# Kernel optimization log

Measured on AMD Instinct MI355X. Metric: run time of the kernel, lower is better.

The kernel has to match this reference:

```python
import jax, jax.numpy as jnp
import numpy as np

# ---- configuration (matches init_kwargs) ----
B, C_IO, T = 2, 64, 4096
PATCH = 2
W0, W1 = 512, 1024           # widths
D_DN, D_MID = 2, 4           # depths per level
DH = 64                      # dim per head
WIN = 128                    # local attention window
MAP = 1024                   # mapping_dim
DFF_MAP = 1024               # mapping_d_ff
FF_MULT = 2                  # GEGLU ff_mult in local levels
H_DN = W0 // DH              # 8 heads
H_MID = W1 // DH             # 16 heads


def _n(key, shape, s=0.02):
    return jax.random.normal(key, shape, jnp.float32) * s


def setup_inputs() -> dict:
    key = jax.random.key(0)
    ks = iter(jax.random.split(key, 64))
    p = {}
    p['x'] = jax.random.normal(next(ks), (B, C_IO, T), jnp.float32)
    p['t'] = jax.random.uniform(next(ks), (B,), jnp.float32)
    p['time_w'] = jax.random.normal(next(ks), (MAP // 2, 1), jnp.float32)
    p['time_in_w'] = _n(next(ks), (MAP, MAP))
    p['map_in_s'] = jnp.ones((MAP,), jnp.float32)
    p['map_norm_s'] = jnp.ones((2, MAP), jnp.float32)
    p['map_up_w'] = _n(next(ks), (2, MAP, 2 * DFF_MAP))
    p['map_down_w'] = _n(next(ks), (2, DFF_MAP, MAP))
    p['map_out_s'] = jnp.ones((MAP,), jnp.float32)
    p['patch_in_w'] = _n(next(ks), (C_IO * PATCH, W0))
    p['dn_anorm_w'] = _n(next(ks), (D_DN, MAP, W0))
    p['dn_qkv_w'] = _n(next(ks), (D_DN, W0, 3 * W0))
    p['dn_o_w'] = _n(next(ks), (D_DN, W0, W0))
    p['dn_fnorm_w'] = _n(next(ks), (D_DN, MAP, W0))
    p['dn_ff1_w'] = _n(next(ks), (D_DN, W0, 2 * FF_MULT * W0))
    p['dn_ff2_w'] = _n(next(ks), (D_DN, FF_MULT * W0, W0))
    p['merge_w'] = _n(next(ks), (W0 * 2, W1))
    p['mid_map_w'] = _n(next(ks), (MAP, W1))
    p['mid_pin_w'] = _n(next(ks), (W1, W1))
    p['mid_pout_w'] = _n(next(ks), (W1, W1))
    p['mid_ln1_g'] = jnp.ones((D_MID, W1), jnp.float32)
    p['mid_ln1_b'] = jnp.zeros((D_MID, W1), jnp.float32)
    p['mid_qkv_w'] = _n(next(ks), (D_MID, W1, 3 * W1))
    p['mid_o_w'] = _n(next(ks), (D_MID, W1, W1))
    p['mid_ln2_g'] = jnp.ones((D_MID, W1), jnp.float32)
    p['mid_ln2_b'] = jnp.zeros((D_MID, W1), jnp.float32)
    p['mid_ff1_w'] = _n(next(ks), (D_MID, W1, 8 * W1))
    p['mid_ff2_w'] = _n(next(ks), (D_MID, 4 * W1, W1))
    p['mid_fn_g'] = jnp.ones((W1,), jnp.float32)
    p['mid_fn_b'] = jnp.zeros((W1,), jnp.float32)
    p['split_w'] = _n(next(ks), (W1, W0 * 2))
    p['split_fac'] = jnp.full((1,), 0.5, jnp.float32)
    p['up_anorm_w'] = _n(next(ks), (D_DN, MAP, W0))
    p['up_qkv_w'] = _n(next(ks), (D_DN, W0, 3 * W0))
    p['up_o_w'] = _n(next(ks), (D_DN, W0, W0))
    p['up_fnorm_w'] = _n(next(ks), (D_DN, MAP, W0))
    p['up_ff1_w'] = _n(next(ks), (D_DN, W0, 2 * FF_MULT * W0))
    p['up_ff2_w'] = _n(next(ks), (D_DN, FF_MULT * W0, W0))
    p['out_norm_s'] = jnp.ones((W0,), jnp.float32)
    p['patch_out_w'] = _n(next(ks), (W0, C_IO * PATCH))
    return p


def rmsnorm(x, scale, eps=1e-6):
    ms = jnp.mean(jnp.square(x), -1, keepdims=True)
    return x * (scale * jax.lax.rsqrt(ms + eps))


def layernorm(x, g, b, eps=1e-5):
    m = jnp.mean(x, -1, keepdims=True)
    v = jnp.mean(jnp.square(x - m), -1, keepdims=True)
    return (x - m) * jax.lax.rsqrt(v + eps) * g + b


def rope_tables(S, D):
    inv = 1.0 / (10000.0 ** (jnp.arange(0, D, 2, dtype=jnp.float32) / D))
    ang = jnp.arange(S, dtype=jnp.float32)[:, None] * inv  # [S, D/2]
    return jnp.cos(ang), jnp.sin(ang)


def apply_rope(x, cos, sin):
    # x: [B,H,S,D], contiguous-half rotation
    x1, x2 = jnp.split(x, 2, -1)
    return jnp.concatenate([x1 * cos - x2 * sin, x2 * cos + x1 * sin], -1)


def heads_split(x, h):
    Bx, S, C = x.shape
    return x.reshape(Bx, S, h, C // h).transpose(0, 2, 1, 3)


def heads_merge(x):
    Bx, h, S, D = x.shape
    return x.transpose(0, 2, 1, 3).reshape(Bx, S, h * D)


def local_attn(q, k, v, w):
    # non-causal sliding-window attention: each query window attends to
    # [prev, self, next] windows (look_backward=1, look_forward=1)
    Bx, H, S, D = q.shape
    nw = S // w
    qw = q.reshape(Bx, H, nw, w, D)
    def ctx(tn):
        tw = tn.reshape(Bx, H, nw, w, D)
        pad = jnp.pad(tw, ((0, 0), (0, 0), (1, 1), (0, 0), (0, 0)))
        return jnp.concatenate([pad[:, :, :-2], pad[:, :, 1:-1], pad[:, :, 2:]], 3)  # [B,H,nw,3w,D]
    kw, vw = ctx(k), ctx(v)
    s = jnp.einsum('bhnqd,bhnkd->bhnqk', qw * (D ** -0.5), kw)
    valid = jnp.ones((nw, 3 * w), bool).at[0, :w].set(False).at[-1, 2 * w:].set(False)
    s = jnp.where(valid[None, None, :, None, :], s, jnp.finfo(s.dtype).min)
    a = jax.nn.softmax(s, -1)
    return jnp.einsum('bhnqk,bhnkd->bhnqd', a, vw).reshape(Bx, H, S, D)


def token_merge(x, w, r=2):
    # 'b (n r) c -> b n (c r)' then linear
    Bx, S, C = x.shape
    x = x.reshape(Bx, S // r, r, C).transpose(0, 1, 3, 2).reshape(Bx, S // r, C * r)
    return x @ w


def token_split(x, w, r=2):
    # linear then 'b n (c r) -> b (n r) c'
    y = x @ w
    Bx, n, CR = y.shape
    C = CR // r
    return y.reshape(Bx, n, C, r).transpose(0, 1, 3, 2).reshape(Bx, n * r, C)


def mapping(e, in_s, norm_s, up_w, down_w, out_s):
    x = rmsnorm(e, in_s)
    for l in range(up_w.shape[0]):
        h = rmsnorm(x, norm_s[l])
        a, g = jnp.split(h @ up_w[l], 2, -1)
        x = x + (a * jax.nn.gelu(g)) @ down_w[l]
    return rmsnorm(x, out_s)


def local_level(x, cond, anorm, qkv_w, o_w, fnorm, ff1, ff2, heads, win):
    Bx, S, C = x.shape
    D = C // heads
    cos, sin = rope_tables(S, D)
    for l in range(qkv_w.shape[0]):
        h = rmsnorm(x, 1.0 + (cond @ anorm[l])[:, None, :])  # AdaRMSNorm
        q, k, v = jnp.split(h @ qkv_w[l], 3, -1)
        q, k, v = heads_split(q, heads), heads_split(k, heads), heads_split(v, heads)
        q, k = apply_rope(q, cos, sin), apply_rope(k, cos, sin)
        x = x + heads_merge(local_attn(q, k, v, win)) @ o_w[l]
        h = rmsnorm(x, 1.0 + (cond @ fnorm[l])[:, None, :])
        a, g = jnp.split(h @ ff1[l], 2, -1)
        x = x + (a * jax.nn.gelu(g)) @ ff2[l]  # GEGLU FF
    return x


def mid_level(x, ln1g, ln1b, qkv_w, o_w, ln2g, ln2b, ff1, ff2, fng, fnb, heads):
    Bx, S, C = x.shape
    D = C // heads
    cos, sin = rope_tables(S, D)
    for l in range(qkv_w.shape[0]):
        h = layernorm(x, ln1g[l], ln1b[l])
        q, k, v = jnp.split(h @ qkv_w[l], 3, -1)
        q, k, v = heads_split(q, heads), heads_split(k, heads), heads_split(v, heads)
        q, k = apply_rope(q, cos, sin), apply_rope(k, cos, sin)
        s = jnp.einsum('bhqd,bhkd->bhqk', q * (D ** -0.5), k)
        o = jnp.einsum('bhqk,bhkd->bhqd', jax.nn.softmax(s, -1), v)
        x = x + heads_merge(o) @ o_w[l]
        h = layernorm(x, ln2g[l], ln2b[l])
        a, g = jnp.split(h @ ff1[l], 2, -1)
        x = x + (a * jax.nn.silu(g)) @ ff2[l]  # SwiGLU FF
    return layernorm(x, fng, fnb)


def _forward(x, t, time_w, time_in_w, map_in_s, map_norm_s, map_up_w, map_down_w, map_out_s,
             patch_in_w, dn_anorm_w, dn_qkv_w, dn_o_w, dn_fnorm_w, dn_ff1_w, dn_ff2_w,
             merge_w, mid_map_w, mid_pin_w, mid_pout_w, mid_ln1_g, mid_ln1_b, mid_qkv_w,
             mid_o_w, mid_ln2_g, mid_ln2_b, mid_ff1_w, mid_ff2_w, mid_fn_g, mid_fn_b,
             split_w, split_fac, up_anorm_w, up_qkv_w, up_o_w, up_fnorm_w, up_ff1_w,
             up_ff2_w, out_norm_s, patch_out_w):
    h = jnp.swapaxes(x, 1, 2)                      # [B,T,C_io]
    h = token_merge(h, patch_in_w, PATCH)          # [B, T/2, W0]
    f = 2.0 * jnp.pi * (t[:, None] @ time_w.T)     # Fourier features
    temb = jnp.concatenate([jnp.cos(f), jnp.sin(f)], -1) @ time_in_w
    cond = mapping(temb, map_in_s, map_norm_s, map_up_w, map_down_w, map_out_s)  # [B,MAP]
    h = local_level(h, cond, dn_anorm_w, dn_qkv_w, dn_o_w, dn_fnorm_w, dn_ff1_w, dn_ff2_w, H_DN, WIN)
    skip = h
    h = token_merge(h, merge_w)                    # [B, T/4, W1]
    h = h @ mid_pin_w
    pre = (cond @ mid_map_w)[:, None, :]           # prepended mapping token
    h = jnp.concatenate([pre, h], 1)
    h = mid_level(h, mid_ln1_g, mid_ln1_b, mid_qkv_w, mid_o_w, mid_ln2_g, mid_ln2_b,
                  mid_ff1_w, mid_ff2_w, mid_fn_g, mid_fn_b, H_MID)
    h = (h @ mid_pout_w)[:, 1:, :]
    h = token_split(h, split_w)                    # back to [B, T/2, W0]
    h = skip + split_fac * (h - skip)              # lerp skip fusion
    h = local_level(h, cond, up_anorm_w, up_qkv_w, up_o_w, up_fnorm_w, up_ff1_w, up_ff2_w, H_DN, WIN)
    h = rmsnorm(h, out_norm_s)
    h = token_split(h, patch_out_w, PATCH)         # [B,T,C_io]
    return jnp.swapaxes(h, 1, 2)


def reference(x, t, time_w, time_in_w, map_in_s, map_norm_s, map_up_w, map_down_w, map_out_s,
              patch_in_w, dn_anorm_w, dn_qkv_w, dn_o_w, dn_fnorm_w, dn_ff1_w, dn_ff2_w,
              merge_w, mid_map_w, mid_pin_w, mid_pout_w, mid_ln1_g, mid_ln1_b, mid_qkv_w,
              mid_o_w, mid_ln2_g, mid_ln2_b, mid_ff1_w, mid_ff2_w, mid_fn_g, mid_fn_b,
              split_w, split_fac, up_anorm_w, up_qkv_w, up_o_w, up_fnorm_w, up_ff1_w,
              up_ff2_w, out_norm_s, patch_out_w):
    return _forward(x, t, time_w, time_in_w, map_in_s, map_norm_s, map_up_w, map_down_w, map_out_s,
                    patch_in_w, dn_anorm_w, dn_qkv_w, dn_o_w, dn_fnorm_w, dn_ff1_w, dn_ff2_w,
                    merge_w, mid_map_w, mid_pin_w, mid_pout_w, mid_ln1_g, mid_ln1_b, mid_qkv_w,
                    mid_o_w, mid_ln2_g, mid_ln2_b, mid_ff1_w, mid_ff2_w, mid_fn_g, mid_fn_b,
                    split_w, split_fac, up_anorm_w, up_qkv_w, up_o_w, up_fnorm_w, up_ff1_w,
                    up_ff2_w, out_norm_s, patch_out_w)
```

## Files before the change

### kernel.cpp

```cpp
#include <hip/hip_runtime.h>
#include <math.h>

#define BB   2
#define CIO  64
#define TT   4096
#define S0   2048
#define W0   512
#define HDN  8
#define SM   1025
#define SMP  1088
#define W1   1024
#define HMID 16
#define WIN  128
#define NW   16
#define MAPD 1024
#define KSPL 16
#define PKCAP 8396800L

typedef _Float16 f16;
typedef _Float16 half8 __attribute__((ext_vector_type(8)));
typedef _Float16 half4v __attribute__((ext_vector_type(4)));
typedef _Float16 half2v __attribute__((ext_vector_type(2)));
typedef float floatx4 __attribute__((ext_vector_type(4)));

__device__ __forceinline__ float gelu_tanh(float x) {
    float x3 = x * x * x;
    return 0.5f * x * (1.f + tanhf(0.7978845608028654f * (x + 0.044715f * x3)));
}

__global__ __launch_bounds__(256) void wcast(
    const float* __restrict__ W, f16* __restrict__ Wt, int K, int N) {
    __shared__ float T[64][65];
    const int n0 = blockIdx.x * 64, k0 = blockIdx.y * 64;
    const int tid = threadIdx.x;
    for (int e = tid; e < 4096; e += 256) {
        int r = e >> 6, c = e & 63;
        T[r][c] = W[(size_t)(k0 + r) * N + n0 + c];
    }
    __syncthreads();
    for (int e = tid; e < 2048; e += 256) {
        int r = e >> 5, c2 = (e & 31) * 2;
        half2v p;
        p[0] = (f16)T[c2][r];
        p[1] = (f16)T[c2 + 1][r];
        *(half2v*)(Wt + (size_t)(n0 + r) * K + k0 + c2) = p;
    }
}

template<int OUTM>
__global__ __launch_bounds__(256) void gemm_h(
    const f16* __restrict__ A, const f16* __restrict__ Bt,
    const float* __restrict__ res, void* __restrict__ Cv,
    int M, int N, int K) {
    __shared__ __align__(16) f16 As[3][4096];
    __shared__ __align__(16) f16 Bs[3][4096];
    const int tid = threadIdx.x;
    const int wv = tid >> 6, ln = tid & 63;
    int nwg = gridDim.x * gridDim.y;
    int orig = blockIdx.y * gridDim.x + blockIdx.x;
    int wg = orig;
    if (nwg >= 16) {
        int q = nwg >> 3, r = nwg & 7;
        int xcd = orig & 7, lot = orig >> 3;
        wg = (xcd < r ? xcd * (q + 1) : r * (q + 1) + (xcd - r) * q) + lot;
    }
    const int bm = (wg / gridDim.x) * 128, bn = (wg % gridDim.x) * 128;
    int Kc = K, kbase = 0;
    if (OUTM == 2) { Kc = K / gridDim.z; kbase = blockIdx.z * Kc; }
    const int nt = Kc >> 5;

    auto stage = [&](int buf, int kt) {
        int k0 = kbase + (kt << 5);
#pragma unroll
        for (int i = 0; i < 2; ++i) {
            int off = i * 4096 + wv * 1024 + ln * 16;
            int row = off >> 6, kb = (off & 63) >> 1;
            int gr = bm + row; gr = gr < M ? gr : M - 1;
            f16* gp = const_cast<f16*>(A) + (size_t)gr * K + k0 + kb;
            __builtin_amdgcn_global_load_lds(
                (__attribute__((address_space(1))) void*)gp,
                (__attribute__((address_space(3))) void*)(&As[buf][i * 2048 + wv * 512]),
                16, 0, 0);
            f16* gq = const_cast<f16*>(Bt) + (size_t)(bn + row) * K + k0 + kb;
            __builtin_amdgcn_global_load_lds(
                (__attribute__((address_space(1))) void*)gq,
                (__attribute__((address_space(3))) void*)(&Bs[buf][i * 2048 + wv * 512]),
                16, 0, 0);
        }
    };

    floatx4 acc[4][4];
#pragma unroll
    for (int m = 0; m < 4; ++m)
#pragma unroll
        for (int n = 0; n < 4; ++n) acc[m][n] = (floatx4)0.f;
    const int r = ln & 15, kc = (ln >> 4) * 8;
    const int wr = (wv >> 1) * 64, wc = (wv & 1) * 64;

    stage(0, 0);
    if (nt > 1) stage(1, 1);
    int buf = 0;
    for (int t = 0; t < nt; ++t) {
        if (t + 1 < nt) { asm volatile("s_waitcnt vmcnt(4)" ::: "memory"); }
        else            { asm volatile("s_waitcnt vmcnt(0)" ::: "memory"); }
        __builtin_amdgcn_s_barrier();
        if (t + 2 < nt) {
            int nb = buf + 2; if (nb >= 3) nb -= 3;
            stage(nb, t + 2);
        }
        half8 af[4], bf[4];
#pragma unroll
        for (int m = 0; m < 4; ++m)
            af[m] = *(const half8*)(&As[buf][(wr + m * 16 + r) * 32 + kc]);
#pragma unroll
        for (int n = 0; n < 4; ++n)
            bf[n] = *(const half8*)(&Bs[buf][(wc + n * 16 + r) * 32 + kc]);
#pragma unroll
        for (int m = 0; m < 4; ++m)
#pragma unroll
            for (int n = 0; n < 4; ++n)
                acc[m][n] = __builtin_amdgcn_mfma_f32_16x16x32_f16(af[m], bf[n], acc[m][n], 0, 0, 0);
        if (++buf >= 3) buf = 0;
    }

    float* Cf = (float*)Cv;
    f16*   Ch = (f16*)Cv;
    if (OUTM == 2) Cf += (size_t)blockIdx.z * M * N;
#pragma unroll
    for (int m = 0; m < 4; ++m) {
        int rbase = bm + wr + m * 16 + ((ln >> 4) << 2);
#pragma unroll
        for (int j = 0; j < 4; ++j) {
            int row = rbase + j;
            if (row < M) {
                size_t ro = (size_t)row * N;
#pragma unroll
                for (int n = 0; n < 4; ++n) {
                    int col = bn + wc + n * 16 + (ln & 15);
                    float v = acc[m][n][j];
                    if (OUTM == 1) Ch[ro + col] = (f16)v;
                    else if (OUTM == 0) Cf[ro + col] = v + (res ? res[ro + col] : 0.f);
                    else Cf[ro + col] = v;
                }
            }
        }
    }
}

template<bool HOUT>
__global__ __launch_bounds__(256) void kred(
    const float* __restrict__ P, const float* __restrict__ res,
    void* __restrict__ Cv, size_t mn, int ks) {
    size_t i = ((size_t)blockIdx.x * 256 + threadIdx.x) * 4;
    if (i >= mn) return;
    floatx4 s = res ? *(const floatx4*)(res + i) : (floatx4)0.f;
    for (int z = 0; z < ks; ++z) {
        floatx4 p = *(const floatx4*)(P + (size_t)z * mn + i);
        s += p;
    }
    if (HOUT) {
        half4v h;
#pragma unroll
        for (int j = 0; j < 4; ++j) h[j] = (f16)s[j];
        *(half4v*)((f16*)Cv + i) = h;
    } else {
        *(floatx4*)((float*)Cv + i) = s;
    }
}

__global__ __launch_bounds__(256) void gemv2_part(
    const float* __restrict__ A, const float* __restrict__ W,
    float* __restrict__ P, int N, int K) {
    int n = blockIdx.x * 256 + threadIdx.x;
    if (n >= N) return;
    int Kc = K / KSPL;
    int k0 = blockIdx.y * Kc;
    float acc0 = 0.f, acc1 = 0.f;
    const float* Wp = W + (size_t)k0 * N + n;
    const float* a0 = A + k0;
    const float* a1 = A + K + k0;
#pragma unroll 4
    for (int k = 0; k < Kc; ++k) {
        float w = Wp[(size_t)k * N];
        acc0 = fmaf(a0[k], w, acc0);
        acc1 = fmaf(a1[k], w, acc1);
    }
    P[((size_t)blockIdx.y * 2 + 0) * N + n] = acc0;
    P[((size_t)blockIdx.y * 2 + 1) * N + n] = acc1;
}

__global__ __launch_bounds__(256) void gemv2_red(
    const float* __restrict__ P, const float* __restrict__ res,
    float* __restrict__ C, int N) {
    int g = blockIdx.x * 256 + threadIdx.x;
    if (g >= 2 * N) return;
    int m = g / N, n = g - m * N;
    float s = res ? res[g] : 0.f;
#pragma unroll
    for (int ky = 0; ky < KSPL; ++ky)
        s += P[((size_t)ky * 2 + m) * N + n];
    C[g] = s;
}

__device__ __forceinline__ void stf(float* p, float v) { *p = v; }
__device__ __forceinline__ void stf(f16* p, float v)   { *p = (f16)v; }

template<typename TO>
__global__ __launch_bounds__(256) void rmsnorm_k(
    const float* __restrict__ X, const float* __restrict__ scale,
    TO* __restrict__ Y, int C, int rows_per_group, float sadd) {
    int row = blockIdx.x, tid = threadIdx.x;
    const float* x = X + (size_t)row * C;
    float v[8];
    int cnt = C >> 8;
    float ss = 0.f;
    for (int i = 0; i < cnt; ++i) { v[i] = x[tid + (i << 8)]; ss += v[i] * v[i]; }
    __shared__ float red[256];
    red[tid] = ss; __syncthreads();
    for (int s2 = 128; s2; s2 >>= 1) { if (tid < s2) red[tid] += red[tid + s2]; __syncthreads(); }
    float inv = rsqrtf(red[0] / (float)C + 1e-6f);
    const float* sc = scale + (size_t)(row / rows_per_group) * C;
    TO* y = Y + (size_t)row * C;
    for (int i = 0; i < cnt; ++i) {
        int c = tid + (i << 8);
        stf(&y[c], v[i] * (sadd + sc[c]) * inv);
    }
}

__global__ __launch_bounds__(256) void layernorm_k(
    const float* __restrict__ X, const float* __restrict__ g,
    const float* __restrict__ bta, f16* __restrict__ Y, int C) {
    int row = blockIdx.x, tid = threadIdx.x;
    const float* x = X + (size_t)row * C;
    float v[8];
    int cnt = C >> 8;
    float s = 0.f;
    for (int i = 0; i < cnt; ++i) { v[i] = x[tid + (i << 8)]; s += v[i]; }
    __shared__ float red[256];
    red[tid] = s; __syncthreads();
    for (int s2 = 128; s2; s2 >>= 1) { if (tid < s2) red[tid] += red[tid + s2]; __syncthreads(); }
    float m = red[0] / (float)C;
    __syncthreads();
    float s2s = 0.f;
    for (int i = 0; i < cnt; ++i) { float d = v[i] - m; s2s += d * d; }
    red[tid] = s2s; __syncthreads();
    for (int s2 = 128; s2; s2 >>= 1) { if (tid < s2) red[tid] += red[tid + s2]; __syncthreads(); }
    float inv = rsqrtf(red[0] / (float)C + 1e-5f);
    f16* y = Y + (size_t)row * C;
    for (int i = 0; i < cnt; ++i) {
        int c = tid + (i << 8);
        y[c] = (f16)((v[i] - m) * inv * g[c] + bta[c]);
    }
}

__global__ __launch_bounds__(256) void glu_k(
    const float* __restrict__ U, float* __restrict__ Yo,
    size_t total, int F, int mode) {
    size_t gidx = (size_t)blockIdx.x * 256 + threadIdx.x;
    if (gidx >= total) return;
    size_t r = gidx / (size_t)F;
    int c = (int)(gidx - r * F);
    const float* u = U + r * (size_t)(2 * F);
    float a = u[c], gg = u[F + c];
    float act = (mode == 0) ? gelu_tanh(gg) : gg / (1.f + expf(-gg));
    Yo[gidx] = a * act;
}

__global__ __launch_bounds__(256) void glu_h8(
    const f16* __restrict__ U, f16* __restrict__ Yo,
    size_t total8, int F8, int mode) {
    size_t gi = (size_t)blockIdx.x * 256 + threadIdx.x;
    if (gi >= total8) return;
    size_t r = gi / (size_t)F8;
    int c = (int)(gi - r * (size_t)F8);
    const f16* u = U + r * (size_t)F8 * 16;
    half8 av = *(const half8*)(u + c * 8);
    half8 gv = *(const half8*)(u + F8 * 8 + c * 8);
    half8 y;
#pragma unroll
    for (int j = 0; j < 8; ++j) {
        float a = (float)av[j], gg = (float)gv[j];
        float act = (mode == 0) ? gelu_tanh(gg) : gg / (1.f + __expf(-gg));
        y[j] = (f16)(a * act);
    }
    *(half8*)(Yo + gi * 8) = y;
}

__global__ __launch_bounds__(256) void qkv_split_rope(
    const f16* __restrict__ QKV, f16* __restrict__ Qo,
    f16* __restrict__ Ko, f16* __restrict__ Vo, int S, int H) {
    int g = blockIdx.x * 256 + threadIdx.x;
    int total = BB * S * H * 32;
    if (g >= total) return;
    int i = g & 31;
    int tix = g >> 5;
    int h = tix % H; tix /= H;
    int s = tix % S; int b = tix / S;
    int C = H * 64;
    const f16* base = QKV + (size_t)(b * S + s) * 3 * C + h * 64;
    float q1 = (float)base[i], q2 = (float)base[32 + i];
    float k1 = (float)base[C + i], k2 = (float)base[C + 32 + i];
    f16 v1 = base[2 * C + i], v2 = base[2 * C + 32 + i];
    float inv = expf(-(float)i * 0.28782313662425575f);
    float ang = (float)s * inv;
    float sn, cs;
    sincosf(ang, &sn, &cs);
    size_t o = ((size_t)(b * H + h) * S + s) * 64 + i;
    Qo[o]      = (f16)((q1 * cs - q2 * sn) * 0.125f);
    Qo[o + 32] = (f16)((q2 * cs + q1 * sn) * 0.125f);
    Ko[o]      = (f16)(k1 * cs - k2 * sn);
    Ko[o + 32] = (f16)(k2 * cs + k1 * sn);
    Vo[o]      = v1;
    Vo[o + 32] = v2;
}

__global__ __launch_bounds__(256) void vtrans(
    const f16* __restrict__ V, f16* __restrict__ Vt, int S, int Spad) {
    __shared__ f16 T[64][72];
    const int tid = threadIdx.x;
    const int k0 = blockIdx.x * 64;
    const f16* Vb = V + (size_t)blockIdx.y * S * 64;
    f16* Vtb = Vt + (size_t)blockIdx.y * 64 * Spad;
    for (int c = tid; c < 512; c += 256) {
        int kk = c >> 3, d8 = (c & 7) * 8;
        int kg = k0 + kk; kg = kg < S ? kg : S - 1;
        half8 v = *(const half8*)(Vb + (size_t)kg * 64 + d8);
        if (k0 + kk >= S) {
#pragma unroll
            for (int j = 0; j < 8; ++j) v[j] = (f16)0.f;
        }
        *(half8*)(&T[kk][d8]) = v;
    }
    __syncthreads();
    for (int c = tid; c < 512; c += 256) {
        int d = c >> 3, k8 = (c & 7) * 8;
        half8 o;
#pragma unroll
        for (int j = 0; j < 8; ++j) o[j] = T[k8 + j][d];
        *(half8*)(Vtb + (size_t)d * Spad + k0 + k8) = o;
    }
}

__global__ __launch_bounds__(256) void fattn(
    const f16* __restrict__ Q, const f16* __restrict__ K,
    const f16* __restrict__ Vt, float* __restrict__ Op,
    float* __restrict__ Mst, float* __restrict__ Lst,
    int S, int Spad, int H, int win, int QR) {
    __shared__ __align__(16) f16 Ks[64][72];
    __shared__ __align__(16) f16 Vs[64][72];
    __shared__ __align__(16) f16 Ps[4][32][72];
    const int tid = threadIdx.x;
    const int wv = tid >> 6, ln = tid & 63;
    const int r15 = ln & 15, g = ln >> 4;
    const int bh = blockIdx.y;
    const int NBH = gridDim.y;
    const int z = blockIdx.z, nz = gridDim.z;
    const int q0 = (int)blockIdx.x * 128;
    const f16* Qb = Q + (size_t)bh * S * 64;
    const f16* Kb = K + (size_t)bh * S * 64;
    const f16* Vtb = Vt + (size_t)bh * 64 * Spad;

    half8 aq[2][2];
#pragma unroll
    for (int m = 0; m < 2; ++m) {
        int q = q0 + wv * 32 + m * 16 + r15;
        q = q < S ? q : S - 1;
#pragma unroll
        for (int ks = 0; ks < 2; ++ks)
            aq[m][ks] = *(const half8*)(Qb + (size_t)q * 64 + ks * 32 + g * 8);
    }
    floatx4 o[2][4];
#pragma unroll
    for (int m = 0; m < 2; ++m)
#pragma unroll
        for (int n = 0; n < 4; ++n) o[m][n] = (floatx4)0.f;
    float mst[2][4], lst[2][4];
#pragma unroll
    for (int m = 0; m < 2; ++m)
#pragma unroll
        for (int j = 0; j < 4; ++j) { mst[m][j] = -3.0e38f; lst[m][j] = 0.f; }

    int klo = 0, khi = S;
    if (win) {
        int n = (int)blockIdx.x;
        klo = (n - 1) * win; if (klo < 0) klo = 0;
        khi = (n + 2) * win; if (khi > S) khi = S;
    }
    int ntile = (khi - klo + 63) >> 6;
    int chunk = (ntile + nz - 1) / nz;
    int myLo = klo + z * chunk * 64;
    int myHi = klo + (z + 1) * chunk * 64; if (myHi > khi) myHi = khi;

    for (int kb = myLo; kb < myHi; kb += 64) {
        __syncthreads();
#pragma unroll
        for (int i = 0; i < 2; ++i) {
            int c = tid + i * 256;
            int rr = c >> 3, c8 = (c & 7) * 8;
            int kg = kb + rr; kg = kg < S ? kg : S - 1;
            *(half8*)(&Ks[rr][c8]) = *(const half8*)(Kb + (size_t)kg * 64 + c8);
            *(half8*)(&Vs[rr][c8]) = *(const half8*)(Vtb + (size_t)rr * Spad + kb + c8);
        }
        __syncthreads();
        floatx4 s[2][4];
#pragma unroll
        for (int m = 0; m < 2; ++m)
#pragma unroll
            for (int n = 0; n < 4; ++n) s[m][n] = (floatx4)0.f;
#pragma unroll
        for (int ks = 0; ks < 2; ++ks) {
            half8 bk[4];
#pragma unroll
            for (int n = 0; n < 4; ++n)
                bk[n] = *(const half8*)(&Ks[n * 16 + r15][ks * 32 + g * 8]);
#pragma unroll
            for (int m = 0; m < 2; ++m)
#pragma unroll
                for (int n = 0; n < 4; ++n)
                    s[m][n] = __builtin_amdgcn_mfma_f32_16x16x32_f16(aq[m][ks], bk[n], s[m][n], 0, 0, 0);
        }
        if (kb + 64 > S) {
#pragma unroll
            for (int n = 0; n < 4; ++n)
                if (kb + n * 16 + r15 >= S) {
#pragma unroll
                    for (int m = 0; m < 2; ++m) s[m][n] = (floatx4)(-3.0e38f);
                }
        }
#pragma unroll
        for (int m = 0; m < 2; ++m) {
#pragma unroll
            for (int j = 0; j < 4; ++j) {
                float tm = fmaxf(fmaxf(s[m][0][j], s[m][1][j]), fmaxf(s[m][2][j], s[m][3][j]));
                tm = fmaxf(tm, __shfl_xor(tm, 1));
                tm = fmaxf(tm, __shfl_xor(tm, 2));
                tm = fmaxf(tm, __shfl_xor(tm, 4));
                tm = fmaxf(tm, __shfl_xor(tm, 8));
                float mn = fmaxf(mst[m][j], tm);
                float sc = __expf(mst[m][j] - mn);
                mst[m][j] = mn;
                float ts = 0.f;
#pragma unroll
                for (int n = 0; n < 4; ++n) {
                    float p = __expf(s[m][n][j] - mn);
                    s[m][n][j] = p;
                    ts += p;
                }
                ts += __shfl_xor(ts, 1);
                ts += __shfl_xor(ts, 2);
                ts += __shfl_xor(ts, 4);
                ts += __shfl_xor(ts, 8);
                lst[m][j] = lst[m][j] * sc + ts;
#pragma unroll
                for (int n = 0; n < 4; ++n) o[m][n][j] *= sc;
            }
        }
#pragma unroll
        for (int m = 0; m < 2; ++m)
#pragma unroll
            for (int n = 0; n < 4; ++n)
#pragma unroll
                for (int j = 0; j < 4; ++j)
                    Ps[wv][m * 16 + g * 4 + j][n * 16 + r15] = (f16)s[m][n][j];
#pragma unroll
        for (int ks = 0; ks < 2; ++ks) {
            half8 pa[2], bv[4];
#pragma unroll
            for (int m = 0; m < 2; ++m)
                pa[m] = *(const half8*)(&Ps[wv][m * 16 + r15][ks * 32 + g * 8]);
#pragma unroll
            for (int n = 0; n < 4; ++n)
                bv[n] = *(const half8*)(&Vs[n * 16 + r15][ks * 32 + g * 8]);
#pragma unroll
            for (int m = 0; m < 2; ++m)
#pragma unroll
                for (int n = 0; n < 4; ++n)
                    o[m][n] = __builtin_amdgcn_mfma_f32_16x16x32_f16(pa[m], bv[n], o[m][n], 0, 0, 0);
        }
    }
    size_t zb = ((size_t)z * NBH + bh) * QR;
#pragma unroll
    for (int m = 0; m < 2; ++m)
#pragma unroll
        for (int j = 0; j < 4; ++j) {
            int qr = q0 + wv * 32 + m * 16 + g * 4 + j;
            size_t ro = (zb + qr) * 64;
#pragma unroll
            for (int n = 0; n < 4; ++n)
                Op[ro + n * 16 + r15] = o[m][n][j];
            if (r15 == 0) {
                Mst[zb + qr] = mst[m][j];
                Lst[zb + qr] = lst[m][j];
            }
        }
}

__global__ __launch_bounds__(256) void fcomb(
    const float* __restrict__ Op, const float* __restrict__ Mst,
    const float* __restrict__ Lst, f16* __restrict__ O,
    int S, int H, int QR, int nz, int rows) {
    int g = blockIdx.x * 256 + threadIdx.x;
    int idx = g >> 4;
    int d4 = (g & 15) * 4;
    if (idx >= rows) return;
    int bh = idx / QR, q = idx - bh * QR;
    if (q >= S) return;
    float mstar = -3.0e38f;
    for (int z = 0; z < nz; ++z)
        mstar = fmaxf(mstar, Mst[(size_t)z * rows + idx]);
    float den = 0.f;
    floatx4 num = (floatx4)0.f;
    for (int z = 0; z < nz; ++z) {
        float w = __expf(Mst[(size_t)z * rows + idx] - mstar);
        den += w * Lst[(size_t)z * rows + idx];
        floatx4 ov = *(const floatx4*)(Op + ((size_t)z * rows + idx) * 64 + d4);
        num += w * ov;
    }
    float inv = 1.f / den;
    int b = bh / H, h = bh % H;
    f16* op = O + ((size_t)b * S + q) * (H * 64) + h * 64 + d4;
    half4v hv;
#pragma unroll
    for (int j = 0; j < 4; ++j) hv[j] = (f16)(num[j] * inv);
    *(half4v*)op = hv;
}

__global__ __launch_bounds__(256) void patch_in_gather(
    const float* __restrict__ x, f16* __restrict__ out) {
    int g = blockIdx.x * 256 + threadIdx.x;
    if (g >= BB * S0 * 128) return;
    int k = g & 127;
    int n = (g >> 7) & (S0 - 1);
    int b = g >> 18;
    out[g] = (f16)x[(size_t)b * CIO * TT + (size_t)(k >> 1) * TT + 2 * n + (k & 1)];
}

__global__ __launch_bounds__(256) void time_embed(
    const float* __restrict__ t, const float* __restrict__ tw,
    float* __restrict__ te) {
    int g = blockIdx.x * 256 + threadIdx.x;
    if (g >= BB * MAPD) return;
    int b = g / MAPD, j = g % MAPD;
    float w = tw[(j < 512) ? j : j - 512];
    float ang = 6.283185307179586f * t[b] * w;
    te[g] = (j < 512) ? cosf(ang) : sinf(ang);
}

__global__ __launch_bounds__(256) void token_merge_gather(
    const float* __restrict__ A, f16* __restrict__ out) {
    int g = blockIdx.x * 256 + threadIdx.x;
    if (g >= BB * 1024 * 1024) return;
    int k = g & 1023;
    int n = (g >> 10) & 1023;
    int b = g >> 20;
    out[g] = (f16)A[((size_t)b * S0 + 2 * n + (k & 1)) * W0 + (k >> 1)];
}

__global__ __launch_bounds__(256) void concat_mid(
    const float* __restrict__ pre, const float* __restrict__ Dsrc,
    float* __restrict__ Cm) {
    int g = blockIdx.x * 256 + threadIdx.x;
    if (g >= BB * SM * W1) return;
    int c = g & 1023;
    int row = g >> 10;
    int b = row / SM, r = row % SM;
    Cm[g] = (r == 0) ? pre[b * W1 + c]
                     : Dsrc[((size_t)b * 1024 + r - 1) * W1 + c];
}

__global__ __launch_bounds__(256) void gather_drop(
    const f16* __restrict__ Dsrc, f16* __restrict__ out) {
    int g = blockIdx.x * 256 + threadIdx.x;
    if (g >= BB * 1024 * W1) return;
    int c = g & 1023;
    int n = (g >> 10) & 1023;
    int b = g >> 20;
    out[g] = Dsrc[((size_t)b * SM + 1 + n) * W1 + c];
}

__global__ __launch_bounds__(256) void split_scatter_lerp(
    const float* __restrict__ y, const float* __restrict__ skip,
    const float* __restrict__ fac, float* __restrict__ xo) {
    int g = blockIdx.x * 256 + threadIdx.x;
    if (g >= BB * S0 * W0) return;
    int c = g & 511;
    int tk = (g >> 9) & (S0 - 1);
    int b = g >> 20;
    float yv = y[((size_t)b * 1024 + (tk >> 1)) * W1 + (c * 2 + (tk & 1))];
    float sk = skip[g];
    xo[g] = sk + fac[0] * (yv - sk);
}

__global__ __launch_bounds__(256) void patch_out_scatter(
    const float* __restrict__ y, float* __restrict__ out) {
    int g = blockIdx.x * 256 + threadIdx.x;
    if (g >= BB * CIO * TT) return;
    int tk = g & (TT - 1);
    int c = (g >> 12) & 63;
    int b = g >> 18;
    out[g] = y[((size_t)b * S0 + (tk >> 1)) * 128 + (c * 2 + (tk & 1))];
}

extern "C" void kernel_launch(void* const* d_in, const int* in_sizes, int n_in,
                              void* d_out, int out_size, void* d_ws, size_t ws_size,
                              hipStream_t stream) {
    const float* x          = (const float*)d_in[0];
    const float* t          = (const float*)d_in[1];
    const float* time_w     = (const float*)d_in[2];
    const float* time_in_w  = (const float*)d_in[3];
    const float* map_in_s   = (const float*)d_in[4];
    const float* map_norm_s = (const float*)d_in[5];
    const float* map_up_w   = (const float*)d_in[6];
    const float* map_down_w = (const float*)d_in[7];
    const float* map_out_s  = (const float*)d_in[8];
    const float* patch_in_w = (const float*)d_in[9];
    const float* dn_anorm_w = (const float*)d_in[10];
    const float* dn_qkv_w   = (const float*)d_in[11];
    const float* dn_o_w     = (const float*)d_in[12];
    const float* dn_fnorm_w = (const float*)d_in[13];
    const float* dn_ff1_w   = (const float*)d_in[14];
    const float* dn_ff2_w   = (const float*)d_in[15];
    const float* merge_w    = (const float*)d_in[16];
    const float* mid_map_w  = (const float*)d_in[17];
    const float* mid_pin_w  = (const float*)d_in[18];
    const float* mid_pout_w = (const float*)d_in[19];
    const float* mid_ln1_g  = (const float*)d_in[20];
    const float* mid_ln1_b  = (const float*)d_in[21];
    const float* mid_qkv_w  = (const float*)d_in[22];
    const float* mid_o_w    = (const float*)d_in[23];
    const float* mid_ln2_g  = (const float*)d_in[24];
    const float* mid_ln2_b  = (const float*)d_in[25];
    const float* mid_ff1_w  = (const float*)d_in[26];
    const float* mid_ff2_w  = (const float*)d_in[27];
    const float* mid_fn_g   = (const float*)d_in[28];
    const float* mid_fn_b   = (const float*)d_in[29];
    const float* split_w    = (const float*)d_in[30];
    const float* split_fac  = (const float*)d_in[31];
    const float* up_anorm_w = (const float*)d_in[32];
    const float* up_qkv_w   = (const float*)d_in[33];
    const float* up_o_w     = (const float*)d_in[34];
    const float* up_fnorm_w = (const float*)d_in[35];
    const float* up_ff1_w   = (const float*)d_in[36];
    const float* up_ff2_w   = (const float*)d_in[37];
    const float* out_norm_s = (const float*)d_in[38];
    const float* patch_out_w= (const float*)d_in[39];

    float* Wp = (float*)d_ws;
    size_t off = 0;
    auto alloc = [&](size_t n) { float* p = Wp + off; off += n; return p; };
    float* A   = alloc((size_t)4096 * 512);
    float* Bsk = alloc((size_t)4096 * 512);
    float* Cm  = alloc((size_t)2050 * 1024);
    float* Df  = alloc((size_t)2050 * 1024);
    f16*  Fq   = (f16*)alloc((size_t)1049600);
    f16*  Fk   = (f16*)alloc((size_t)1049600);
    f16*  Fv   = (f16*)alloc((size_t)1049600);
    f16*  Fvt  = (f16*)alloc((size_t)1114112);
    f16*  H1   = (f16*)alloc((size_t)8396800);
    f16*  H2   = (f16*)alloc((size_t)4198400);
    f16*  Wh   = (f16*)alloc((size_t)4194304);
    float* Pk  = alloc((size_t)PKCAP);
    float* ML  = alloc((size_t)262144);
    float* Pb  = alloc((size_t)KSPL * 2 * 2048);
    float* Sma = alloc((size_t)32768);
    (void)ws_size; (void)in_sizes; (void)n_in; (void)out_size;

    float* te   = Sma;
    float* temb = Sma + 2048;
    float* mapx = Sma + 4096;
    float* maph = Sma + 6144;
    float* mapu = Sma + 8192;
    float* mapg = Sma + 12288;
    float* cond = Sma + 14336;
    float* sA   = Sma + 16384;
    float* sF   = Sma + 17408;
    float* pre  = Sma + 18432;

    auto WC = [&](const float* W, int K, int N) {
        wcast<<<dim3(N / 64, K / 64), 256, 0, stream>>>(W, Wh, K, N);
    };
    auto pick_ks = [](int M, int N, int K) {
        long gx = N / 128, gy = (M + 127) / 128;
        int ks = 1;
        while (gx * gy * ks < 512 && ks < 8) {
            int nk = ks * 2;
            if ((K / nk) % 32 != 0 || (long)M * N * nk > PKCAP) break;
            ks = nk;
        }
        return ks;
    };
    auto GF = [&](const f16* Aa, const float* res, float* C, int M, int N, int K) {
        int ks = pick_ks(M, N, K);
        dim3 g(N / 128, (M + 127) / 128, ks);
        if (ks == 1) {
            gemm_h<0><<<g, 256, 0, stream>>>(Aa, Wh, res, C, M, N, K);
        } else {
            gemm_h<2><<<g, 256, 0, stream>>>(Aa, Wh, nullptr, Pk, M, N, K);
            size_t mn = (size_t)M * N;
            kred<false><<<(int)((mn / 4 + 255) / 256), 256, 0, stream>>>(Pk, res, C, mn, ks);
        }
    };
    auto GH = [&](const f16* Aa, f16* C, int M, int N, int K) {
        int ks = pick_ks(M, N, K);
        dim3 g(N / 128, (M + 127) / 128, ks);
        if (ks == 1) {
            gemm_h<1><<<g, 256, 0, stream>>>(Aa, Wh, nullptr, C, M, N, K);
        } else {
            gemm_h<2><<<g, 256, 0, stream>>>(Aa, Wh, nullptr, Pk, M, N, K);
            size_t mn = (size_t)M * N;
            kred<true><<<(int)((mn / 4 + 255) / 256), 256, 0, stream>>>(Pk, nullptr, C, mn, ks);
        }
    };
    auto gemv2 = [&](const float* Aa, const float* W, const float* res,
                     float* C, int N, int K) {
        gemv2_part<<<dim3((N + 255) / 256, KSPL), 256, 0, stream>>>(Aa, W, Pb, N, K);
        gemv2_red<<<(2 * N + 255) / 256, 256, 0, stream>>>(Pb, res, C, N);
    };
    auto FATT = [&](const f16* Qp, const f16* Kp, const f16* Vtp, f16* Out,
                    int S, int Spad, int H, int win, int nq, int nbh, int nz) {
        int QR = nq * 128;
        int rows = nbh * QR;
        fattn<<<dim3(nq, nbh, nz), 256, 0, stream>>>(
            Qp, Kp, Vtp, Pk, ML, ML + (size_t)nz * rows, S, Spad, H, win, QR);
        fcomb<<<(rows * 16 + 255) / 256, 256, 0, stream>>>(
            Pk, ML, ML + (size_t)nz * rows, Out, S, H, QR, nz, rows);
    };

    patch_in_gather<<<(BB * S0 * 128 + 255) / 256, 256, 0, stream>>>(x, H2);
    WC(patch_in_w, 128, 512);
    GF(H2, nullptr, A, 4096, 512, 128);

    time_embed<<<(BB * MAPD + 255) / 256, 256, 0, stream>>>(t, time_w, te);
    gemv2(te, time_in_w, nullptr, temb, 1024, 1024);
    rmsnorm_k<float><<<2, 256, 0, stream>>>(temb, map_in_s, mapx, 1024, 2, 0.f);
    for (int l = 0; l < 2; ++l) {
        rmsnorm_k<float><<<2, 256, 0, stream>>>(mapx, map_norm_s + (size_t)l * 1024, maph, 1024, 2, 0.f);
        gemv2(maph, map_up_w + (size_t)l * 1024 * 2048, nullptr, mapu, 2048, 1024);
        glu_k<<<(2 * 1024 + 255) / 256, 256, 0, stream>>>(mapu, mapg, 2 * 1024, 1024, 0);
        gemv2(mapg, map_down_w + (size_t)l * 1024 * 1024, mapx, mapx, 1024, 1024);
    }
    rmsnorm_k<float><<<2, 256, 0, stream>>>(mapx, map_out_s, cond, 1024, 2, 0.f);

    auto run_local = [&](const float* anorm, const float* qkvw, const float* ow,
                         const float* fnorm, const float* ff1, const float* ff2) {
        for (int l = 0; l < 2; ++l) {
            gemv2(cond, anorm + (size_t)l * 1024 * 512, nullptr, sA, 512, 1024);
            rmsnorm_k<f16><<<4096, 256, 0, stream>>>(A, sA, H2, 512, 2048, 1.f);
            WC(qkvw + (size_t)l * 512 * 1536, 512, 1536);
            GH(H2, H1, 4096, 1536, 512);
            qkv_split_rope<<<(BB * S0 * HDN * 32 + 255) / 256, 256, 0, stream>>>(H1, Fq, Fk, Fv, S0, HDN);
            vtrans<<<dim3(S0 / 64, BB * HDN), 256, 0, stream>>>(Fv, Fvt, S0, S0);
            FATT(Fq, Fk, Fvt, H2, S0, S0, HDN, WIN, S0 / 128, BB * HDN, 2);
            WC(ow + (size_t)l * 512 * 512, 512, 512);
            GF(H2, A, A, 4096, 512, 512);
            gemv2(cond, fnorm + (size_t)l * 1024 * 512, nullptr, sF, 512, 1024);
            rmsnorm_k<f16><<<4096, 256, 0, stream>>>(A, sF, H2, 512, 2048, 1.f);
            WC(ff1 + (size_t)l * 512 * 2048, 512, 2048);
            GH(H2, H1, 4096, 2048, 512);
            glu_h8<<<(4096 * 128 + 255) / 256, 256, 0, stream>>>(H1, H2, (size_t)4096 * 128, 128, 0);
            WC(ff2 + (size_t)l * 1024 * 512, 1024, 512);
            GF(H2, A, A, 4096, 512, 1024);
        }
    };
    run_local(dn_anorm_w, dn_qkv_w, dn_o_w, dn_fnorm_w, dn_ff1_w, dn_ff2_w);

    hipMemcpyAsync(Bsk, A, (size_t)4096 * 512 * 4, hipMemcpyDeviceToDevice, stream);
    token_merge_gather<<<(BB * 1024 * 1024 + 255) / 256, 256, 0, stream>>>(A, H2);
    WC(merge_w, 1024, 1024);
    GH(H2, H1, 2048, 1024, 1024);
    WC(mid_pin_w, 1024, 1024);
    GF(H1, nullptr, Df, 2048, 1024, 1024);
    gemv2(cond, mid_map_w, nullptr, pre, 1024, 1024);
    concat_mid<<<(BB * SM * W1 + 255) / 256, 256, 0, stream>>>(pre, Df, Cm);

    for (int l = 0; l < 4; ++l) {
        layernorm_k<<<2050, 256, 0, stream>>>(Cm, mid_ln1_g + (size_t)l * 1024,
                                              mid_ln1_b + (size_t)l * 1024, H2, 1024);
        WC(mid_qkv_w + (size_t)l * 1024 * 3072, 1024, 3072);
        GH(H2, H1, 2050, 3072, 1024);
        qkv_split_rope<<<(BB * SM * HMID * 32 + 255) / 256, 256, 0, stream>>>(H1, Fq, Fk, Fv, SM, HMID);
        vtrans<<<dim3(SMP / 64, BB * HMID), 256, 0, stream>>>(Fv, Fvt, SM, SMP);
        FATT(Fq, Fk, Fvt, H2, SM, SMP, HMID, 0, 9, BB * HMID, 3);
        WC(mid_o_w + (size_t)l * 1024 * 1024, 1024, 1024);
        GF(H2, Cm, Cm, 2050, 1024, 1024);
        layernorm_k<<<2050, 256, 0, stream>>>(Cm, mid_ln2_g + (size_t)l * 1024,
                                              mid_ln2_b + (size_t)l * 1024, H2, 1024);
        WC(mid_ff1_w + (size_t)l * 1024 * 8192, 1024, 8192);
        GH(H2, H1, 2050, 8192, 1024);
        glu_h8<<<(int)(((size_t)2050 * 512 + 255) / 256), 256, 0, stream>>>(H1, H2, (size_t)2050 * 512, 512, 1);
        WC(mid_ff2_w + (size_t)l * 4096 * 1024, 4096, 1024);
        GF(H2, Cm, Cm, 2050, 1024, 4096);
    }
    layernorm_k<<<2050, 256, 0, stream>>>(Cm, mid_fn_g, mid_fn_b, H2, 1024);

    WC(mid_pout_w, 1024, 1024);
    GH(H2, H1, 2050, 1024, 1024);
    gather_drop<<<(BB * 1024 * W1 + 255) / 256, 256, 0, stream>>>(H1, H2);
    WC(split_w, 1024, 1024);
    GF(H2, nullptr, Df, 2048, 1024, 1024);
    split_scatter_lerp<<<(BB * S0 * W0 + 255) / 256, 256, 0, stream>>>(Df, Bsk, split_fac, A);

    run_local(up_anorm_w, up_qkv_w, up_o_w, up_fnorm_w, up_ff1_w, up_ff2_w);

    rmsnorm_k<f16><<<4096, 256, 0, stream>>>(A, out_norm_s, H2, 512, 4096, 0.f);
    WC(patch_out_w, 512, 128);
    GF(H2, nullptr, Df, 4096, 128, 512);
    patch_out_scatter<<<(BB * CIO * TT + 255) / 256, 256, 0, stream>>>(Df, (float*)d_out);
}
```

Measured before the change: 2.110 ms.

## Fuse RoPE and QKV head split into QKV GEMM epilogue; batch conditioning GEMVs

```diff
diff --git a/kernel.cpp b/kernel.cpp
--- a/kernel.cpp
+++ b/kernel.cpp
@@ -147,6 +147,130 @@
     }
 }
 
+__global__ __launch_bounds__(256) void gemm_qkv(
+    const f16* __restrict__ A, const f16* __restrict__ Bt,
+    const float* __restrict__ tab, f16* __restrict__ Fq,
+    f16* __restrict__ Fk, f16* __restrict__ Fv,
+    int M, int N, int K, int S, int H) {
+    __shared__ __align__(16) f16 As[3][4096];
+    __shared__ __align__(16) f16 Bs[3][4096];
+    const int tid = threadIdx.x;
+    const int wv = tid >> 6, ln = tid & 63;
+    int nwg = gridDim.x * gridDim.y;
+    int orig = blockIdx.y * gridDim.x + blockIdx.x;
+    int wg = orig;
+    if (nwg >= 16) {
+        int q = nwg >> 3, r = nwg & 7;
+        int xcd = orig & 7, lot = orig >> 3;
+        wg = (xcd < r ? xcd * (q + 1) : r * (q + 1) + (xcd - r) * q) + lot;
+    }
+    const int bm = (wg / gridDim.x) * 128, bn = (wg % gridDim.x) * 128;
+    const int nt = K >> 5;
+
+    auto stage = [&](int buf, int kt) {
+        int k0 = kt << 5;
+#pragma unroll
+        for (int i = 0; i < 2; ++i) {
+            int off = i * 4096 + wv * 1024 + ln * 16;
+            int row = off >> 6, kb = (off & 63) >> 1;
+            int gr = bm + row; gr = gr < M ? gr : M - 1;
+            f16* gp = const_cast<f16*>(A) + (size_t)gr * K + k0 + kb;
+            __builtin_amdgcn_global_load_lds(
+                (__attribute__((address_space(1))) void*)gp,
+                (__attribute__((address_space(3))) void*)(&As[buf][i * 2048 + wv * 512]),
+                16, 0, 0);
+            f16* gq = const_cast<f16*>(Bt) + (size_t)(bn + row) * K + k0 + kb;
+            __builtin_amdgcn_global_load_lds(
+                (__attribute__((address_space(1))) void*)gq,
+                (__attribute__((address_space(3))) void*)(&Bs[buf][i * 2048 + wv * 512]),
+                16, 0, 0);
+        }
+    };
+
+    floatx4 acc[4][4];
+#pragma unroll
+    for (int m = 0; m < 4; ++m)
+#pragma unroll
+        for (int n = 0; n < 4; ++n) acc[m][n] = (floatx4)0.f;
+    const int r = ln & 15, kc = (ln >> 4) * 8;
+    const int wr = (wv >> 1) * 64, wc = (wv & 1) * 64;
+
+    stage(0, 0);
+    if (nt > 1) stage(1, 1);
+    int buf = 0;
+    for (int t = 0; t < nt; ++t) {
+        if (t + 1 < nt) { asm volatile("s_waitcnt vmcnt(4)" ::: "memory"); }
+        else            { asm volatile("s_waitcnt vmcnt(0)" ::: "memory"); }
+        __builtin_amdgcn_s_barrier();
+        if (t + 2 < nt) {
+            int nb = buf + 2; if (nb >= 3) nb -= 3;
+            stage(nb, t + 2);
+        }
+        half8 af[4], bf[4];
+#pragma unroll
+        for (int m = 0; m < 4; ++m)
+            af[m] = *(const half8*)(&As[buf][(wr + m * 16 + r) * 32 + kc]);
+#pragma unroll
+        for (int n = 0; n < 4; ++n)
+            bf[n] = *(const half8*)(&Bs[buf][(wc + n * 16 + r) * 32 + kc]);
+#pragma unroll
+        for (int m = 0; m < 4; ++m)
+#pragma unroll
+            for (int n = 0; n < 4; ++n)
+                acc[m][n] = __builtin_amdgcn_mfma_f32_16x16x32_f16(af[m], bf[n], acc[m][n], 0, 0, 0);
+        if (++buf >= 3) buf = 0;
+    }
+
+    const int C = N / 3;
+    const int colbase = bn + wc;
+    const int reg = colbase / C;
+    const int h = (colbase % C) >> 6;
+#pragma unroll
+    for (int m = 0; m < 4; ++m) {
+        int rbase = bm + wr + m * 16 + ((ln >> 4) << 2);
+#pragma unroll
+        for (int j = 0; j < 4; ++j) {
+            int row = rbase + j;
+            if (row >= M) continue;
+            int b = row / S, s = row - b * S;
+            size_t ob = ((size_t)(b * H + h) * S + s) * 64;
+            if (reg == 2) {
+#pragma unroll
+                for (int n = 0; n < 4; ++n)
+                    Fv[ob + n * 16 + (ln & 15)] = (f16)acc[m][n][j];
+            } else {
+                const float* tb = tab + ((size_t)s << 6);
+#pragma unroll
+                for (int p = 0; p < 2; ++p) {
+                    int i = p * 16 + (ln & 15);
+                    float cs = tb[2 * i], sn = tb[2 * i + 1];
+                    float x1 = acc[m][p][j], x2 = acc[m][p + 2][j];
+                    float o1 = x1 * cs - x2 * sn;
+                    float o2 = x2 * cs + x1 * sn;
+                    if (reg == 0) {
+                        Fq[ob + i]      = (f16)(o1 * 0.125f);
+                        Fq[ob + i + 32] = (f16)(o2 * 0.125f);
+                    } else {
+                        Fk[ob + i]      = (f16)o1;
+                        Fk[ob + i + 32] = (f16)o2;
+                    }
+                }
+            }
+        }
+    }
+}
+
+__global__ __launch_bounds__(256) void rope_tab(float* __restrict__ tab, int S) {
+    int g = blockIdx.x * 256 + threadIdx.x;
+    if (g >= S * 32) return;
+    int s = g >> 5, i = g & 31;
+    float inv = expf(-(float)i * 0.28782313662425575f);
+    float sn, cs;
+    sincosf((float)s * inv, &sn, &cs);
+    tab[2 * g] = cs;
+    tab[2 * g + 1] = sn;
+}
+
 template<bool HOUT>
 __global__ __launch_bounds__(256) void kred(
     const float* __restrict__ P, const float* __restrict__ res,
@@ -200,6 +324,43 @@
     for (int ky = 0; ky < KSPL; ++ky)
         s += P[((size_t)ky * 2 + m) * N + n];
     C[g] = s;
+}
+
+__global__ __launch_bounds__(256) void gemv2L_part(
+    const float* __restrict__ A, const float* __restrict__ W,
+    float* __restrict__ P, int Nper, int L, int K) {
+    int tot = L * Nper;
+    int c = blockIdx.x * 256 + threadIdx.x;
+    if (c >= tot) return;
+    int l = c / Nper, n = c - l * Nper;
+    int Kc = K / KSPL;
+    int k0 = blockIdx.y * Kc;
+    const float* Wp = W + (size_t)l * K * Nper + (size_t)k0 * Nper + n;
+    const float* a0 = A + k0;
+    const float* a1 = A + K + k0;
+    float acc0 = 0.f, acc1 = 0.f;
+#pragma unroll 4
+    for (int k = 0; k < Kc; ++k) {
+        float w = Wp[(size_t)k * Nper];
+        acc0 = fmaf(a0[k], w, acc0);
+        acc1 = fmaf(a1[k], w, acc1);
+    }
+    P[((size_t)blockIdx.y * 2 + 0) * tot + c] = acc0;
+    P[((size_t)blockIdx.y * 2 + 1) * tot + c] = acc1;
+}
+
+__global__ __launch_bounds__(256) void gemv2L_red(
+    const float* __restrict__ P, float* __restrict__ C, int Nper, int L) {
+    int tot = L * Nper;
+    int g = blockIdx.x * 256 + threadIdx.x;
+    if (g >= 2 * tot) return;
+    int m = g / tot, cc = g - m * tot;
+    float s = 0.f;
+#pragma unroll
+    for (int ky = 0; ky < KSPL; ++ky)
+        s += P[((size_t)ky * 2 + m) * tot + cc];
+    int l = cc / Nper, n = cc - l * Nper;
+    C[((size_t)l * 2 + m) * Nper + n] = s;
 }
 
 __device__ __forceinline__ void stf(float* p, float v) { *p = v; }
@@ -284,34 +445,6 @@
         y[j] = (f16)(a * act);
     }
     *(half8*)(Yo + gi * 8) = y;
-}
-
-__global__ __launch_bounds__(256) void qkv_split_rope(
-    const f16* __restrict__ QKV, f16* __restrict__ Qo,
-    f16* __restrict__ Ko, f16* __restrict__ Vo, int S, int H) {
-    int g = blockIdx.x * 256 + threadIdx.x;
-    int total = BB * S * H * 32;
-    if (g >= total) return;
-    int i = g & 31;
-    int tix = g >> 5;
-    int h = tix % H; tix /= H;
-    int s = tix % S; int b = tix / S;
-    int C = H * 64;
-    const f16* base = QKV + (size_t)(b * S + s) * 3 * C + h * 64;
-    float q1 = (float)base[i], q2 = (float)base[32 + i];
-    float k1 = (float)base[C + i], k2 = (float)base[C + 32 + i];
-    f16 v1 = base[2 * C + i], v2 = base[2 * C + 32 + i];
-    float inv = expf(-(float)i * 0.28782313662425575f);
-    float ang = (float)s * inv;
-    float sn, cs;
-    sincosf(ang, &sn, &cs);
-    size_t o = ((size_t)(b * H + h) * S + s) * 64 + i;
-    Qo[o]      = (f16)((q1 * cs - q2 * sn) * 0.125f);
-    Qo[o + 32] = (f16)((q2 * cs + q1 * sn) * 0.125f);
-    Ko[o]      = (f16)(k1 * cs - k2 * sn);
-    Ko[o + 32] = (f16)(k2 * cs + k1 * sn);
-    Vo[o]      = v1;
-    Vo[o + 32] = v2;
 }
 
 __global__ __launch_bounds__(256) void vtrans(
@@ -648,21 +781,23 @@
     float* Wp = (float*)d_ws;
     size_t off = 0;
     auto alloc = [&](size_t n) { float* p = Wp + off; off += n; return p; };
-    float* A   = alloc((size_t)4096 * 512);
-    float* Bsk = alloc((size_t)4096 * 512);
-    float* Cm  = alloc((size_t)2050 * 1024);
-    float* Df  = alloc((size_t)2050 * 1024);
-    f16*  Fq   = (f16*)alloc((size_t)1049600);
-    f16*  Fk   = (f16*)alloc((size_t)1049600);
-    f16*  Fv   = (f16*)alloc((size_t)1049600);
-    f16*  Fvt  = (f16*)alloc((size_t)1114112);
-    f16*  H1   = (f16*)alloc((size_t)8396800);
-    f16*  H2   = (f16*)alloc((size_t)4198400);
-    f16*  Wh   = (f16*)alloc((size_t)4194304);
-    float* Pk  = alloc((size_t)PKCAP);
-    float* ML  = alloc((size_t)262144);
-    float* Pb  = alloc((size_t)KSPL * 2 * 2048);
-    float* Sma = alloc((size_t)32768);
+    float* A    = alloc((size_t)4096 * 512);
+    float* Bsk  = alloc((size_t)4096 * 512);
+    float* Cm   = alloc((size_t)2050 * 1024);
+    float* Df   = alloc((size_t)2050 * 1024);
+    f16*  Fq    = (f16*)alloc((size_t)1049600);
+    f16*  Fk    = (f16*)alloc((size_t)1049600);
+    f16*  Fv    = (f16*)alloc((size_t)1049600);
+    f16*  Fvt   = (f16*)alloc((size_t)1114112);
+    f16*  H1    = (f16*)alloc((size_t)8396800);
+    f16*  H2    = (f16*)alloc((size_t)4198400);
+    f16*  Wh    = (f16*)alloc((size_t)4194304);
+    float* Pk   = alloc((size_t)PKCAP);
+    float* ML   = alloc((size_t)262144);
+    float* Pb   = alloc((size_t)KSPL * 2 * 2048);
+    float* tabL = alloc((size_t)S0 * 64);
+    float* tabM = alloc((size_t)SM * 64);
+    float* Sma  = alloc((size_t)32768);
     (void)ws_size; (void)in_sizes; (void)n_in; (void)out_size;
 
     float* te   = Sma;
@@ -672,9 +807,11 @@
     float* mapu = Sma + 8192;
     float* mapg = Sma + 12288;
     float* cond = Sma + 14336;
-    float* sA   = Sma + 16384;
-    float* sF   = Sma + 17408;
     float* pre  = Sma + 18432;
+    float* sAdn = Sma + 20480;
+    float* sFdn = Sma + 22528;
+    float* sAup = Sma + 24576;
+    float* sFup = Sma + 26624;
 
     auto WC = [&](const float* W, int K, int N) {
         wcast<<<dim3(N / 64, K / 64), 256, 0, stream>>>(W, Wh, K, N);
@@ -711,10 +848,19 @@
             kred<true><<<(int)((mn / 4 + 255) / 256), 256, 0, stream>>>(Pk, nullptr, C, mn, ks);
         }
     };
+    auto GQKV = [&](const f16* Aa, const float* tab, int M, int N, int K, int S, int H) {
+        dim3 g(N / 128, (M + 127) / 128);
+        gemm_qkv<<<g, 256, 0, stream>>>(Aa, Wh, tab, Fq, Fk, Fv, M, N, K, S, H);
+    };
     auto gemv2 = [&](const float* Aa, const float* W, const float* res,
                      float* C, int N, int K) {
         gemv2_part<<<dim3((N + 255) / 256, KSPL), 256, 0, stream>>>(Aa, W, Pb, N, K);
         gemv2_red<<<(2 * N + 255) / 256, 256, 0, stream>>>(Pb, res, C, N);
+    };
+    auto gemv2L = [&](const float* Aa, const float* W, float* C, int Nper, int L, int K) {
+        int tot = L * Nper;
+        gemv2L_part<<<dim3((tot + 255) / 256, KSPL), 256, 0, stream>>>(Aa, W, Pb, Nper, L, K);
+        gemv2L_red<<<(2 * tot + 255) / 256, 256, 0, stream>>>(Pb, C, Nper, L);
     };
     auto FATT = [&](const f16* Qp, const f16* Kp, const f16* Vtp, f16* Out,
                     int S, int Spad, int H, int win, int nq, int nbh, int nz) {
@@ -726,6 +872,9 @@
             Pk, ML, ML + (size_t)nz * rows, Out, S, H, QR, nz, rows);
     };
 
+    rope_tab<<<(S0 * 32 + 255) / 256, 256, 0, stream>>>(tabL, S0);
+    rope_tab<<<(SM * 32 + 255) / 256, 256, 0, stream>>>(tabM, SM);
+
     patch_in_gather<<<(BB * S0 * 128 + 255) / 256, 256, 0, stream>>>(x, H2);
     WC(patch_in_w, 128, 512);
     GF(H2, nullptr, A, 4096, 512, 128);
@@ -741,20 +890,24 @@
     }
     rmsnorm_k<float><<<2, 256, 0, stream>>>(mapx, map_out_s, cond, 1024, 2, 0.f);
 
-    auto run_local = [&](const float* anorm, const float* qkvw, const float* ow,
-                         const float* fnorm, const float* ff1, const float* ff2) {
+    gemv2L(cond, dn_anorm_w, sAdn, 512, 2, 1024);
+    gemv2L(cond, dn_fnorm_w, sFdn, 512, 2, 1024);
+    gemv2L(cond, up_anorm_w, sAup, 512, 2, 1024);
+    gemv2L(cond, up_fnorm_w, sFup, 512, 2, 1024);
+    gemv2L(cond, mid_map_w,  pre, 1024, 1, 1024);
+
+    auto run_local = [&](const float* qkvw, const float* ow,
+                         const float* ff1, const float* ff2,
+                         const float* sAall, const float* sFall) {
         for (int l = 0; l < 2; ++l) {
-            gemv2(cond, anorm + (size_t)l * 1024 * 512, nullptr, sA, 512, 1024);
-            rmsnorm_k<f16><<<4096, 256, 0, stream>>>(A, sA, H2, 512, 2048, 1.f);
+            rmsnorm_k<f16><<<4096, 256, 0, stream>>>(A, sAall + (size_t)l * 1024, H2, 512, 2048, 1.f);
             WC(qkvw + (size_t)l * 512 * 1536, 512, 1536);
-            GH(H2, H1, 4096, 1536, 512);
-            qkv_split_rope<<<(BB * S0 * HDN * 32 + 255) / 256, 256, 0, stream>>>(H1, Fq, Fk, Fv, S0, HDN);
+            GQKV(H2, tabL, 4096, 1536, 512, S0, HDN);
             vtrans<<<dim3(S0 / 64, BB * HDN), 256, 0, stream>>>(Fv, Fvt, S0, S0);
             FATT(Fq, Fk, Fvt, H2, S0, S0, HDN, WIN, S0 / 128, BB * HDN, 2);
             WC(ow + (size_t)l * 512 * 512, 512, 512);
             GF(H2, A, A, 4096, 512, 512);
-            gemv2(cond, fnorm + (size_t)l * 1024 * 512, nullptr, sF, 512, 1024);
-            rmsnorm_k<f16><<<4096, 256, 0, stream>>>(A, sF, H2, 512, 2048, 1.f);
+            rmsnorm_k<f16><<<4096, 256, 0, stream>>>(A, sFall + (size_t)l * 1024, H2, 512, 2048, 1.f);
             WC(ff1 + (size_t)l * 512 * 2048, 512, 2048);
             GH(H2, H1, 4096, 2048, 512);
             glu_h8<<<(4096 * 128 + 255) / 256, 256, 0, stream>>>(H1, H2, (size_t)4096 * 128, 128, 0);
@@ -762,7 +915,7 @@
             GF(H2, A, A, 4096, 512, 1024);
         }
     };
-    run_local(dn_anorm_w, dn_qkv_w, dn_o_w, dn_fnorm_w, dn_ff1_w, dn_ff2_w);
+    run_local(dn_qkv_w, dn_o_w, dn_ff1_w, dn_ff2_w, sAdn, sFdn);
 
     hipMemcpyAsync(Bsk, A, (size_t)4096 * 512 * 4, hipMemcpyDeviceToDevice, stream);
     token_merge_gather<<<(BB * 1024 * 1024 + 255) / 256, 256, 0, stream>>>(A, H2);
@@ -770,15 +923,13 @@
     GH(H2, H1, 2048, 1024, 1024);
     WC(mid_pin_w, 1024, 1024);
     GF(H1, nullptr, Df, 2048, 1024, 1024);
-    gemv2(cond, mid_map_w, nullptr, pre, 1024, 1024);
     concat_mid<<<(BB * SM * W1 + 255) / 256, 256, 0, stream>>>(pre, Df, Cm);
 
     for (int l = 0; l < 4; ++l) {
         layernorm_k<<<2050, 256, 0, stream>>>(Cm, mid_ln1_g + (size_t)l * 1024,
                                               mid_ln1_b + (size_t)l * 1024, H2, 1024);
         WC(mid_qkv_w + (size_t)l * 1024 * 3072, 1024, 3072);
-        GH(H2, H1, 2050, 3072, 1024);
-        qkv_split_rope<<<(BB * SM * HMID * 32 + 255) / 256, 256, 0, stream>>>(H1, Fq, Fk, Fv, SM, HMID);
+        GQKV(H2, tabM, 2050, 3072, 1024, SM, HMID);
         vtrans<<<dim3(SMP / 64, BB * HMID), 256, 0, stream>>>(Fv, Fvt, SM, SMP);
         FATT(Fq, Fk, Fvt, H2, SM, SMP, HMID, 0, 9, BB * HMID, 3);
         WC(mid_o_w + (size_t)l * 1024 * 1024, 1024, 1024);
@@ -800,7 +951,7 @@
     GF(H2, nullptr, Df, 2048, 1024, 1024);
     split_scatter_lerp<<<(BB * S0 * W0 + 255) / 256, 256, 0, stream>>>(Df, Bsk, split_fac, A);
 
-    run_local(up_anorm_w, up_qkv_w, up_o_w, up_fnorm_w, up_ff1_w, up_ff2_w);
+    run_local(up_qkv_w, up_o_w, up_ff1_w, up_ff2_w, sAup, sFup);
 
     rmsnorm_k<f16><<<4096, 256, 0, stream>>>(A, out_norm_s, H2, 512, 4096, 0.f);
     WC(patch_out_w, 512, 128);
```

Result: no change. 2.101 ms (-0.4%).
